# Performance work log

Measured on AMD Instinct MI355X. Metric: run time of the kernel, lower is better.

Reference implementation:

```python
import jax, jax.numpy as jnp
import numpy as np

# sarModule stage: in=256, out=512, blocks=2, stride=2, patch_groups=4, mask_size=7
B, C_IN, H, W = 32, 256, 56, 56
C_OUT = 512
PLANES = C_OUT // 4   # Bottleneck inner width = planes // expansion = 128
G = 4                 # patch_groups
MS = 7                # mask_size
TEMP = 1.0            # gumbel-softmax temperature


def conv(x, w, stride=1, pad=0, groups=1):
    return jax.lax.conv_general_dilated(
        x, w, (stride, stride), [(pad, pad), (pad, pad)],
        feature_group_count=groups,
        dimension_numbers=('NCHW', 'OIHW', 'NCHW'))


def bn(x, g, b):
    # BatchNorm in inference form with running_mean=0, running_var=1 folded in
    return x * g[None, :, None, None] + b[None, :, None, None]


def avgpool3s2(x):
    # nn.AvgPool2d(3, stride=2, padding=1), count_include_pad=True
    s = jax.lax.reduce_window(x, 0.0, jax.lax.add, (1, 1, 3, 3), (1, 1, 2, 2),
                              [(0, 0), (0, 0), (1, 1), (1, 1)])
    return s / 9.0


def setup_inputs() -> dict:
    key = jax.random.key(0)
    ks = iter(jax.random.split(key, 64))

    def w(shape):
        fan_in = int(np.prod(shape[1:]))
        return jax.random.normal(next(ks), shape, jnp.float32) * np.float32((2.0 / fan_in) ** 0.5)

    ones = lambda n: jnp.ones((n,), jnp.float32)
    zeros = lambda n: jnp.zeros((n,), jnp.float32)

    x = jax.random.normal(next(ks), (B, C_IN, H, W), jnp.float32)
    u = jax.random.uniform(next(ks), (B, 2, G, MS, MS), jnp.float32, 1e-6, 1.0 - 1e-6)
    gumbel_noise = -jnp.log(-jnp.log(u))

    return dict(
        x=x, gumbel_noise=gumbel_noise,
        # base Bottleneck (256->512, stride 2, downsample = avgpool + 1x1 conv + bn)
        b_w1=w((PLANES, C_IN, 1, 1)), b_g1=ones(PLANES), b_b1=zeros(PLANES),
        b_w2=w((PLANES, PLANES, 3, 3)), b_g2=ones(PLANES), b_b2=zeros(PLANES),
        b_w3=w((C_OUT, PLANES, 1, 1)), b_g3=ones(C_OUT), b_b3=zeros(C_OUT),
        b_dw=w((C_OUT, C_IN, 1, 1)), b_dg=ones(C_OUT), b_db=zeros(C_OUT),
        # refine Bottleneck (256->512, stride 1, downsample = 1x1 conv + bn)
        r_w1=w((PLANES, C_IN, 1, 1)), r_g1=ones(PLANES), r_b1=zeros(PLANES),
        r_w2=w((PLANES, PLANES, 3, 3)), r_g2=ones(PLANES), r_b2=zeros(PLANES),
        r_w3=w((C_OUT, PLANES, 1, 1)), r_g3=ones(C_OUT), r_b3=zeros(C_OUT),
        r_dw=w((C_OUT, C_IN, 1, 1)), r_dg=ones(C_OUT), r_db=zeros(C_OUT),
        # maskGen: grouped 3x3 conv (512 -> 4*G), bn, pool, grouped 1x1 fc (4*G -> 2*G)
        m_w=w((4 * G, C_OUT // G, 3, 3)), m_g=ones(4 * G), m_b=zeros(4 * G),
        m_fcw=w((2 * G, 4, 1, 1)),
        m_fcb=jnp.concatenate([0.1 * ones(G), 5.0 * ones(G)]),  # bias init from maskGen
        # fusion Bottleneck (512->512, stride 2, downsample = avgpool only)
        f_w1=w((PLANES, C_OUT, 1, 1)), f_g1=ones(PLANES), f_b1=zeros(PLANES),
        f_w2=w((PLANES, PLANES, 3, 3)), f_g2=ones(PLANES), f_b2=zeros(PLANES),
        f_w3=w((C_OUT, PLANES, 1, 1)), f_g3=ones(C_OUT), f_b3=zeros(C_OUT),
    )


def reference(x, gumbel_noise,
              b_w1, b_g1, b_b1, b_w2, b_g2, b_b2, b_w3, b_g3, b_b3, b_dw, b_dg, b_db,
              r_w1, r_g1, r_b1, r_w2, r_g2, r_b2, r_w3, r_g3, r_b3, r_dw, r_dg, r_db,
              m_w, m_g, m_b, m_fcw, m_fcb,
              f_w1, f_g1, f_b1, f_w2, f_g2, f_b2, f_w3, f_g3, f_b3):
    # ---- base branch: Bottleneck stride 2, last_relu=False -> [B,512,28,28]
    o = jax.nn.relu(bn(conv(x, b_w1), b_g1, b_b1))
    o = jax.nn.relu(bn(conv(o, b_w2, stride=2, pad=1), b_g2, b_b2))
    o = bn(conv(o, b_w3), b_g3, b_b3)
    x_base = o + bn(conv(avgpool3s2(x), b_dw), b_dg, b_db)

    # ---- maskGen on x_base
    gmap = jax.nn.relu(bn(conv(x_base, m_w, pad=1, groups=G), m_g, m_b))      # [B,16,28,28]
    hb = x_base.shape[2] // MS                                                 # adaptive avgpool 28->7
    gmap = gmap.reshape(B, 4 * G, MS, hb, MS, hb).mean(axis=(3, 5))            # [B,16,7,7]
    logits = conv(gmap, m_fcw, groups=G) + m_fcb[None, :, None, None]          # [B,8,7,7]
    logits = logits.reshape(B, 2, G, MS, MS)                                   # view(B,2,groups,ms,ms)
    # hard gumbel-softmax over dim 1 with straight-through estimator
    y = jax.nn.softmax((logits + gumbel_noise) / TEMP, axis=1)
    hard = jax.nn.one_hot(jnp.argmax(y, axis=1), 2, axis=1, dtype=y.dtype)
    gates = hard + y - jax.lax.stop_gradient(y)
    mask = gates[:, 1]                                                         # [B,G,7,7]

    # nearest-upsample mask x8 and expand across each channel group
    mask_up = jnp.repeat(jnp.repeat(mask, H // MS, axis=-2), W // MS, axis=-1) # [B,G,56,56]
    mask_full = jnp.broadcast_to(mask_up[:, :, None], (B, G, C_OUT // G, H, W)).reshape(B, C_OUT, H, W)

    # ---- refine branch: Bottleneck stride 1, output gated by mask, last_relu=False
    o = jax.nn.relu(bn(conv(x, r_w1), r_g1, r_b1))
    o = jax.nn.relu(bn(conv(o, r_w2, pad=1), r_g2, r_b2))
    o = bn(conv(o, r_w3), r_g3, r_b3) * mask_full
    x_refine = o + bn(conv(x, r_dw), r_dg, r_db)                               # [B,512,56,56]

    # ---- fuse: bilinear upsample base to refine resolution (align_corners=False)
    x_base_up = jax.image.resize(x_base, (B, C_OUT, H, W), 'bilinear')
    fused = jax.nn.relu(x_base_up + x_refine)

    # ---- fusion Bottleneck: stride 2, downsample = avgpool only, last_relu=True
    o = jax.nn.relu(bn(conv(fused, f_w1), f_g1, f_b1))
    o = jax.nn.relu(bn(conv(o, f_w2, stride=2, pad=1), f_g2, f_b2))
    o = bn(conv(o, f_w3), f_g3, f_b3)
    out = jax.nn.relu(o + avgpool3s2(fused))                                   # [B,512,28,28]
    return out, mask
```

## Files before the change

### kernel.cpp

```cpp
#include <hip/hip_runtime.h>
#include <cstdint>

#define BB   32
#define CINX 256
#define HH   56
#define WW   56
#define HWX  3136
#define CO   512
#define PL   128
#define HP   28
#define WP   28
#define HWP  784
#define NG   4
#define MSZ  7

typedef unsigned short ushortT;
typedef unsigned int   uint32;
typedef __attribute__((ext_vector_type(8))) short short8;
typedef __attribute__((ext_vector_type(4))) float f32x4;

__device__ __forceinline__ ushortT f2bf(float f){
  uint32 u = __float_as_uint(f);
  u = (u + 0x7fffu + ((u >> 16) & 1u)) >> 16;
  return (ushortT)u;
}
__device__ __forceinline__ float bf2f(ushortT u){
  return __uint_as_float(((uint32)u) << 16);
}
__device__ __forceinline__ void split2(float v, ushortT& h, ushortT& lo){
  h = f2bf(v);
  lo = f2bf(v - bf2f(h));
}
__device__ __forceinline__ uint32 packu(ushortT a, ushortT b){
  return (uint32)a | ((uint32)b << 16);
}

typedef __attribute__((address_space(1))) const void g_void;
typedef __attribute__((address_space(3))) void l_void;
__device__ __forceinline__ void glds16(const ushortT* g, ushortT* l){
  __builtin_amdgcn_global_load_lds((g_void*)g, (l_void*)l, 16, 0, 0);
}

__device__ __forceinline__ void wsplit(float v, ushortT* dh, ushortT* dl, size_t i){
  ushortT h, lo; split2(v, h, lo); dh[i] = h; dl[i] = lo;
}

__global__ __launch_bounds__(256) void prep_w(
  const float* __restrict__ b_w1, const float* __restrict__ b_g1,
  const float* __restrict__ b_w2, const float* __restrict__ b_g2,
  const float* __restrict__ b_w3, const float* __restrict__ b_g3,
  const float* __restrict__ b_dw, const float* __restrict__ b_dg,
  const float* __restrict__ r_w1, const float* __restrict__ r_g1,
  const float* __restrict__ r_w2, const float* __restrict__ r_g2,
  const float* __restrict__ r_w3, const float* __restrict__ r_g3,
  const float* __restrict__ r_dw, const float* __restrict__ r_dg,
  const float* __restrict__ f_w1, const float* __restrict__ f_g1,
  const float* __restrict__ f_w2, const float* __restrict__ f_g2,
  const float* __restrict__ f_w3, const float* __restrict__ f_g3,
  const float* __restrict__ b_b1, const float* __restrict__ r_b1,
  ushortT* __restrict__ dh, ushortT* __restrict__ dl,
  ushortT* __restrict__ zp, float* __restrict__ biasC)
{
  const int idx = blockIdx.x*256 + threadIdx.x;
  switch (blockIdx.y){
    case 0: {
      if (idx >= 32768) return; int m = idx >> 8;
      wsplit(b_w1[idx]*b_g1[m], dh, dl, (size_t)0 + idx); } break;
    case 3: {
      if (idx >= 32768) return; int m = idx >> 8;
      wsplit(r_w1[idx]*r_g1[m], dh, dl, 32768 + (size_t)idx); } break;
    case 1: {
      if (idx >= 147456) return; int m = idx / 1152; int k = idx - m*1152;
      int tap = k >> 7, c = k & 127;
      wsplit(b_w2[((size_t)(m*128 + c))*9 + tap]*b_g2[m], dh, dl, 65536 + (size_t)idx); } break;
    case 2: {
      if (idx >= 196608) return; int m = idx / 384; int k = idx - m*384;
      float v = (k < 128) ? b_w3[m*128 + k]*b_g3[m] : b_dw[m*256 + (k-128)]*b_dg[m];
      wsplit(v, dh, dl, 212992 + (size_t)idx); } break;
    case 4: {
      if (idx >= 147456) return; int m = idx / 1152; int k = idx - m*1152;
      int tap = k >> 7, c = k & 127;
      wsplit(r_w2[((size_t)(m*128 + c))*9 + tap]*r_g2[m], dh, dl, 409600 + (size_t)idx); } break;
    case 5: {
      if (idx >= 196608) return; int m = idx / 384; int k = idx - m*384;
      float v = (k < 128) ? r_w3[m*128 + k]*r_g3[m] : r_dw[m*256 + (k-128)]*r_dg[m];
      wsplit(v, dh, dl, 557056 + (size_t)idx); } break;
    case 6: {
      if (idx >= 65536) return; int m = idx >> 9;
      wsplit(f_w1[idx]*f_g1[m], dh, dl, 753664 + (size_t)idx); } break;
    case 7: {
      if (idx >= 147456) return; int m = idx / 1152; int k = idx - m*1152;
      int tap = k >> 7, c = k & 127;
      wsplit(f_w2[((size_t)(m*128 + c))*9 + tap]*f_g2[m], dh, dl, 819200 + (size_t)idx); } break;
    case 8: {
      if (idx >= 65536) return; int m = idx >> 7;
      wsplit(f_w3[idx]*f_g3[m], dh, dl, 966656 + (size_t)idx); } break;
    case 9: {
      if (idx < 64) zp[idx] = 0;
      if (idx < 128) biasC[idx] = b_b1[idx];
      else if (idx < 256) biasC[idx] = r_b1[idx-128];
    } break;
  }
}

__global__ __launch_bounds__(256) void k_pool2(const float* __restrict__ x,
    ushortT* __restrict__ ph_, ushortT* __restrict__ pl_){
  __shared__ float s[16][17];
  const int p0 = blockIdx.x*16, c0 = blockIdx.y*16, bz = blockIdx.z;
  const int ci = threadIdx.x >> 4, pi = threadIdx.x & 15;
  {
    const int p = p0 + pi;
    const int oy = p / WP, ox = p - oy*WP;
    const float* src = x + ((size_t)bz*CINX + c0 + ci)*HWX;
    float sum = 0.f;
    #pragma unroll
    for (int dy=0; dy<3; dy++){
      int yy = 2*oy-1+dy;
      if ((unsigned)yy >= HH) continue;
      #pragma unroll
      for (int dx=0; dx<3; dx++){
        int xx = 2*ox-1+dx;
        if ((unsigned)xx >= WW) continue;
        sum += src[yy*WW + xx];
      }
    }
    s[ci][pi] = sum * (1.f/9.f);
  }
  __syncthreads();
  const int pr = threadIdx.x >> 4, cj = threadIdx.x & 15;
  float v = s[cj][pr];
  ushortT h, lo; split2(v, h, lo);
  size_t o = ((size_t)bz*HWP + p0 + pr)*CINX + c0 + cj;
  ph_[o] = h; pl_[o] = lo;
}

__global__ __launch_bounds__(256) void prep_x2(const float* __restrict__ x,
    ushortT* __restrict__ xh, ushortT* __restrict__ xl){
  __shared__ float s[16][17];
  const int p0 = blockIdx.x*16, c0 = blockIdx.y*16, bz = blockIdx.z;
  const int ci = threadIdx.x >> 4, pi = threadIdx.x & 15;
  s[ci][pi] = x[((size_t)bz*CINX + c0 + ci)*HWX + p0 + pi];
  __syncthreads();
  const int pr = threadIdx.x >> 4, cj = threadIdx.x & 15;
  float v = s[cj][pr];
  ushortT h, lo; split2(v, h, lo);
  size_t o = ((size_t)bz*HWX + p0 + pr)*CINX + c0 + cj;
  xh[o] = h; xl[o] = lo;
}

__global__ __launch_bounds__(256) void k_poolf(const ushortT* __restrict__ fzh,
    const ushortT* __restrict__ fzl, float* __restrict__ pf){
  const int pb = blockIdx.x, bz = blockIdx.y;
  const int psub = threadIdx.x >> 6;
  const int lane = threadIdx.x & 63;
  const int p = pb*4 + psub;
  const int oy = p / WP, ox = p - oy*WP;
  const int c = lane*8;
  float s[8] = {0.f,0.f,0.f,0.f,0.f,0.f,0.f,0.f};
  #pragma unroll
  for (int dy=0; dy<3; dy++){
    const int iy = 2*oy - 1 + dy;
    if ((unsigned)iy >= (unsigned)HH) continue;
    #pragma unroll
    for (int dx=0; dx<3; dx++){
      const int ix = 2*ox - 1 + dx;
      if ((unsigned)ix >= (unsigned)WW) continue;
      const size_t fi = ((size_t)bz*HWX + (size_t)(iy*WW + ix))*CO + c;
      uint4 hh = *(const uint4*)(fzh + fi);
      uint4 ll = *(const uint4*)(fzl + fi);
      ushortT hv[8], lv[8];
      *(uint4*)hv = hh; *(uint4*)lv = ll;
      #pragma unroll
      for (int j=0;j<8;j++) s[j] += bf2f(hv[j]) + bf2f(lv[j]);
    }
  }
  const size_t o = ((size_t)bz*HWP + p)*CO + c;
  float4 o0 = make_float4(s[0]*(1.f/9.f), s[1]*(1.f/9.f), s[2]*(1.f/9.f), s[3]*(1.f/9.f));
  float4 o1 = make_float4(s[4]*(1.f/9.f), s[5]*(1.f/9.f), s[6]*(1.f/9.f), s[7]*(1.f/9.f));
  *(float4*)(pf + o)     = o0;
  *(float4*)(pf + o + 4) = o1;
}

template<int KIND,int EPI,int S1F,int MT,int NWV,int DBUF,int SWAP,int GX,int GY,
         int STRIDE,int PAD,int HIN,int WIN,int WOUT,int NOUT,int C1,int C2,
         int BSTR1,int MTOT,int KTOT>
__global__ __launch_bounds__(NWV*64)
void gemm_bf3(const ushortT* __restrict__ wph, const ushortT* __restrict__ wpl,
              const ushortT* __restrict__ s1h, const ushortT* __restrict__ s1l,
              const ushortT* __restrict__ s2h, const ushortT* __restrict__ s2l,
              const float* __restrict__ xf32,
              const float* __restrict__ bias1, const float* __restrict__ bias2,
              const float* __restrict__ maskf, const float* __restrict__ xbase,
              const ushortT* __restrict__ zp,
              ushortT* __restrict__ oh, ushortT* __restrict__ ol,
              float* __restrict__ of32)
{
  constexpr int ACALLS  = MT/(16*NWV);
  constexpr int BCALLS2 = 8/NWV;
  constexpr int GLDS_PER = (ACALLS + BCALLS2)*2;
  constexpr bool GATHER1 = (KIND==0 && S1F==1);
  constexpr int BUFSZ = MT*64 + 8192;
  constexpr int WNs = (MT==256) ? 2 : (NWV==8 ? 4 : 2);
  constexpr int NF  = 128/(WNs*16);
  constexpr int T = GX*GY*BB;
  static_assert(T % 8 == 0, "grid not divisible by 8 XCDs");
  constexpr int QX = T/8;
  __shared__ ushortT smem[BUFSZ*(DBUF+1)];

  const int tid = threadIdx.x;
  const int lin = blockIdx.x;
  const int virt = (lin & 7)*QX + (lin >> 3);
  const int vx = virt % GX;
  const int vrest = virt / GX;
  const int vy = vrest % GY;
  const int bz = vrest / GY;
  const int nt = SWAP ? vy : vx;
  const int mt = SWAP ? vx : vy;
  const int l  = tid & 63, w = tid >> 6;
  const int wm = w / WNs, wn = w % WNs;

  size_t a_src[2]; int a_dst[2];
  #pragma unroll
  for (int c=0;c<ACALLS;c++){
    int s = (w*ACALLS + c)*64 + l;
    int row = s >> 2, slotm = s & 3;
    int logical = slotm ^ ((row >> 1) & 3);
    a_src[c] = (size_t)(mt*MT + row)*KTOT + logical*8;
    a_dst[c] = (w*ACALLS + c)*512;
  }

  int b_dst[2]; size_t b_base1[2], b_base2[2]; int b_klane[2];
  int b_oy[2], b_ox[2]; bool b_ok[2]; float b_mv[2];
  #pragma unroll
  for (int c=0;c<BCALLS2;c++){
    int s = (w*BCALLS2 + c)*64 + l;
    int row = s >> 2, slotm = s & 3;
    int logical = slotm ^ ((row >> 1) & 3);
    b_klane[c] = logical*8;
    b_dst[c] = (w*BCALLS2 + c)*512;
    int ngr = nt*128 + row;
    b_ok[c] = (ngr < NOUT);
    int oyv = ngr / WOUT, oxv = ngr - (ngr / WOUT)*WOUT;
    b_oy[c] = oyv; b_ox[c] = oxv;
    b_base1[c] = ((size_t)bz*NOUT + ngr)*BSTR1 + b_klane[c];
    b_base2[c] = ((size_t)bz*NOUT + ngr)*C2 + b_klane[c];
    b_mv[c] = 1.f;
    if (KIND == 3)
      b_mv[c] = b_ok[c] ? maskf[((size_t)(bz*NG + mt)*MSZ + (oyv>>3))*MSZ + (oxv>>3)] : 0.f;
  }

  const int sr = tid >> 1;
  const int hp = tid & 1;
  const int swz = (sr >> 1) & 3;
  const int lws0 = sr*32 + ((2*hp) ^ swz)*8;
  const int lws1 = sr*32 + ((2*hp + 1) ^ swz)*8;
  const int ng = nt*128 + sr;

  f32x4 acc[4][4];
  f32x4 zf = {0.f,0.f,0.f,0.f};
  #pragma unroll
  for (int i=0;i<4;i++)
    #pragma unroll
    for (int j=0;j<4;j++) acc[i][j] = zf;

  auto stagef = [&](int ks, ushortT* AHb, ushortT* ALb, ushortT* BHb, ushortT* BLb){
    const int k0 = ks*32;
    #pragma unroll
    for (int c=0;c<ACALLS;c++){
      glds16(wph + a_src[c] + k0, AHb + a_dst[c]);
      glds16(wpl + a_src[c] + k0, ALb + a_dst[c]);
    }
    if constexpr (GATHER1){
      if (tid < 256){
        uint4 b0 = make_uint4(0,0,0,0), b1v = b0, b2v = b0, b3v = b0;
        if (ng < NOUT){
          size_t fbase = ((size_t)bz*C1 + k0 + hp*16)*(size_t)NOUT + ng;
          ushortT h[16], lo[16];
          #pragma unroll
          for (int e=0;e<16;e++){ split2(xf32[fbase + (size_t)e*NOUT], h[e], lo[e]); }
          b0  = make_uint4(packu(h[0],h[1]),  packu(h[2],h[3]),  packu(h[4],h[5]),  packu(h[6],h[7]));
          b1v = make_uint4(packu(h[8],h[9]),  packu(h[10],h[11]),packu(h[12],h[13]),packu(h[14],h[15]));
          b2v = make_uint4(packu(lo[0],lo[1]),packu(lo[2],lo[3]),packu(lo[4],lo[5]),packu(lo[6],lo[7]));
          b3v = make_uint4(packu(lo[8],lo[9]),packu(lo[10],lo[11]),packu(lo[12],lo[13]),packu(lo[14],lo[15]));
        }
        *(uint4*)(BHb + lws0) = b0;  *(uint4*)(BHb + lws1) = b1v;
        *(uint4*)(BLb + lws0) = b2v; *(uint4*)(BLb + lws1) = b3v;
      }
    } else {
      #pragma unroll
      for (int c=0;c<BCALLS2;c++){
        const ushortT *sh, *sl;
        if constexpr (KIND == 0){
          bool ok = b_ok[c];
          size_t off = b_base1[c] + k0;
          sh = ok ? s1h + off : zp;  sl = ok ? s1l + off : zp;
        } else if constexpr (KIND == 1){
          const int tap = k0 >> 7;
          const int cb  = (k0 & 127);
          const int dy = tap/3, dx = tap - 3*(tap/3);
          int iy = b_oy[c]*STRIDE + dy - PAD;
          int ix = b_ox[c]*STRIDE + dx - PAD;
          bool ok = b_ok[c] && (unsigned)iy < (unsigned)HIN && (unsigned)ix < (unsigned)WIN;
          size_t off = ((size_t)bz*(HIN*WIN) + (size_t)(iy*WIN + ix))*BSTR1 + cb + b_klane[c];
          sh = ok ? s1h + off : zp;  sl = ok ? s1l + off : zp;
        } else {
          if (k0 < C1){
            bool ok = b_ok[c] && (KIND != 3 || b_mv[c] != 0.f);
            size_t off = b_base1[c] + k0;
            sh = ok ? s1h + off : zp;  sl = ok ? s1l + off : zp;
          } else {
            bool ok = b_ok[c];
            size_t off = b_base2[c] + (k0 - C1);
            sh = ok ? s2h + off : zp;  sl = ok ? s2l + off : zp;
          }
        }
        glds16(sh, BHb + b_dst[c]);
        glds16(sl, BLb + b_dst[c]);
      }
    }
  };

  auto computef = [&](const ushortT* AHb, const ushortT* ALb,
                      const ushortT* BHb, const ushortT* BLb){
    short8 bh[NF], bl[NF];
    #pragma unroll
    for (int nf=0; nf<NF; nf++){
      const int rr = wn*(NF*16) + nf*16 + (l & 15);
      const int ph = (l >> 4) ^ ((rr >> 1) & 3);
      bh[nf] = *(const short8*)(BHb + rr*32 + ph*8);
      bl[nf] = *(const short8*)(BLb + rr*32 + ph*8);
    }
    #pragma unroll
    for (int mf=0; mf<4; mf++){
      const int rr = wm*64 + mf*16 + (l & 15);
      const int ph = (l >> 4) ^ ((rr >> 1) & 3);
      short8 ah = *(const short8*)(AHb + rr*32 + ph*8);
      short8 al = *(const short8*)(ALb + rr*32 + ph*8);
      #pragma unroll
      for (int nf=0; nf<NF; nf++)
        acc[mf][nf] = __builtin_amdgcn_mfma_f32_16x16x32_bf16(ah, bh[nf], acc[mf][nf], 0,0,0);
      #pragma unroll
      for (int nf=0; nf<NF; nf++)
        acc[mf][nf] = __builtin_amdgcn_mfma_f32_16x16x32_bf16(ah, bl[nf], acc[mf][nf], 0,0,0);
      #pragma unroll
      for (int nf=0; nf<NF; nf++)
        acc[mf][nf] = __builtin_amdgcn_mfma_f32_16x16x32_bf16(al, bh[nf], acc[mf][nf], 0,0,0);
    }
  };

  const int NK = KTOT / 32;
  if constexpr (DBUF == 0){
    ushortT* AH  = smem;
    ushortT* AL  = smem + MT*32;
    ushortT* BHs = smem + MT*64;
    ushortT* BLs = smem + MT*64 + 4096;
    for (int ks=0; ks<NK; ks++){
      stagef(ks, AH, AL, BHs, BLs);
      __syncthreads();
      computef(AH, AL, BHs, BLs);
      __syncthreads();
    }
  } else {
    stagef(0, smem, smem + MT*32, smem + MT*64, smem + MT*64 + 4096);
    asm volatile("s_waitcnt vmcnt(0)" ::: "memory");
    __builtin_amdgcn_s_barrier();
    for (int ks=0; ks<NK; ks++){
      ushortT* cb = smem + (ks & 1)*BUFSZ;
      ushortT* nb = smem + ((ks & 1) ^ 1)*BUFSZ;
      if (ks + 1 < NK){
        stagef(ks + 1, nb, nb + MT*32, nb + MT*64, nb + MT*64 + 4096);
        if constexpr (GLDS_PER == 4)
          asm volatile("s_waitcnt vmcnt(4)" ::: "memory");
        else
          asm volatile("s_waitcnt vmcnt(8)" ::: "memory");
      } else {
        asm volatile("s_waitcnt vmcnt(0)" ::: "memory");
      }
      __builtin_amdgcn_sched_barrier(0);
      __builtin_amdgcn_s_barrier();
      computef(cb, cb + MT*32, cb + MT*64, cb + MT*64 + 4096);
      __builtin_amdgcn_s_barrier();
    }
  }

  const int mb0 = mt*MT + wm*64;
  const int nb0 = nt*128 + wn*(NF*16);

  #pragma unroll
  for (int nf=0; nf<NF; nf++){
    const int n = nb0 + nf*16 + (l & 15);
    if (n >= NOUT) continue;
    if constexpr (EPI == 0){
      const size_t ob = ((size_t)bz*NOUT + n)*MTOT;
      #pragma unroll
      for (int mf=0; mf<4; mf++){
        const int m0 = mb0 + mf*16 + (l>>4)*4;
        ushort4 hq, lq; ushortT h0, l0; float v;
        v = fmaxf(acc[mf][nf][0] + bias1[m0+0], 0.f); split2(v,h0,l0); hq.x=h0; lq.x=l0;
        v = fmaxf(acc[mf][nf][1] + bias1[m0+1], 0.f); split2(v,h0,l0); hq.y=h0; lq.y=l0;
        v = fmaxf(acc[mf][nf][2] + bias1[m0+2], 0.f); split2(v,h0,l0); hq.z=h0; lq.z=l0;
        v = fmaxf(acc[mf][nf][3] + bias1[m0+3], 0.f); split2(v,h0,l0); hq.w=h0; lq.w=l0;
        *(ushort4*)(oh + ob + m0) = hq;
        *(ushort4*)(ol + ob + m0) = lq;
      }
    } else if constexpr (EPI == 1){
      #pragma unroll
      for (int mf=0; mf<4; mf++){
        const int m0 = mb0 + mf*16 + (l>>4)*4;
        #pragma unroll
        for (int r=0;r<4;r++){
          const int m = m0 + r;
          of32[((size_t)bz*MTOT + m)*NOUT + n] = acc[mf][nf][r] + bias1[m] + bias2[m];
        }
      }
    } else if constexpr (EPI == 2){
      const int y = n / WOUT, x = n - (n / WOUT)*WOUT;
      const int grpw = (mt*MT + wm*64) >> 7;
      const float mvv = maskf[((size_t)(bz*NG + grpw)*MSZ + (y>>3))*MSZ + (x>>3)];
      const int iy = y >> 1, ix = x >> 1;
      int yA,yB,xA,xB; float wyA,wyB,wxA,wxB;
      if (y & 1){ yA=iy; wyA=0.75f; yB=(iy+1<HP)?iy+1:HP-1; wyB=0.25f; }
      else      { yA=(iy>0)?iy-1:0; wyA=0.25f; yB=iy; wyB=0.75f; }
      if (x & 1){ xA=ix; wxA=0.75f; xB=(ix+1<WP)?ix+1:WP-1; wxB=0.25f; }
      else      { xA=(ix>0)?ix-1:0; wxA=0.25f; xB=ix; wxB=0.75f; }
      const size_t ob = ((size_t)bz*NOUT + n)*MTOT;
      #pragma unroll
      for (int mf=0; mf<4; mf++){
        const int m0 = mb0 + mf*16 + (l>>4)*4;
        ushort4 hq, lq;
        #pragma unroll
        for (int r=0;r<4;r++){
          const int m = m0 + r;
          const float* xb = xbase + ((size_t)bz*MTOT + m)*HWP;
          float up = wyA*(wxA*xb[yA*WP+xA] + wxB*xb[yA*WP+xB])
                   + wyB*(wxA*xb[yB*WP+xA] + wxB*xb[yB*WP+xB]);
          float v = fmaxf(acc[mf][nf][r] + up + mvv*bias1[m] + bias2[m], 0.f);
          ushortT h0, l0; split2(v, h0, l0);
          if      (r==0){hq.x=h0;lq.x=l0;}
          else if (r==1){hq.y=h0;lq.y=l0;}
          else if (r==2){hq.z=h0;lq.z=l0;}
          else          {hq.w=h0;lq.w=l0;}
        }
        *(ushort4*)(oh + ob + m0) = hq;
        *(ushort4*)(ol + ob + m0) = lq;
      }
    } else {
      const float* pfrow = xbase + ((size_t)bz*NOUT + n)*MTOT;
      #pragma unroll
      for (int mf=0; mf<4; mf++){
        const int m0 = mb0 + mf*16 + (l>>4)*4;
        const float4 pv = *(const float4*)(pfrow + m0);
        of32[((size_t)bz*MTOT + m0+0)*NOUT + n] = fmaxf(acc[mf][nf][0] + bias1[m0+0] + pv.x, 0.f);
        of32[((size_t)bz*MTOT + m0+1)*NOUT + n] = fmaxf(acc[mf][nf][1] + bias1[m0+1] + pv.y, 0.f);
        of32[((size_t)bz*MTOT + m0+2)*NOUT + n] = fmaxf(acc[mf][nf][2] + bias1[m0+2] + pv.z, 0.f);
        of32[((size_t)bz*MTOT + m0+3)*NOUT + n] = fmaxf(acc[mf][nf][3] + bias1[m0+3] + pv.w, 0.f);
      }
    }
  }
}

#define GM_LDSW 9216
__global__ __launch_bounds__(256) void k_gmap2(const float* __restrict__ xbase,
    const float* __restrict__ mw, const float* __restrict__ mg, const float* __restrict__ mb,
    float* __restrict__ gmap){
  __shared__ float wsh[GM_LDSW];
  __shared__ float red[16][2][4][16];
  const int tile = blockIdx.x, b = blockIdx.y;
  const int tid = threadIdx.x;
  const int pl = tid & 15, cs = tid >> 4;
  const int p = tile*16 + pl;
  const int oy = p / WP, ox = p - oy*WP;
  int toff[9];
  #pragma unroll
  for (int tap=0; tap<9; tap++){
    int dy = tap/3, dx = tap - 3*dy;
    int yy = oy + dy - 1, xx = ox + dx - 1;
    toff[tap] = ((unsigned)yy < (unsigned)HP && (unsigned)xx < (unsigned)WP) ? (yy*WP + xx) : -1;
  }
  float acc[2][4] = {{0.f,0.f,0.f,0.f},{0.f,0.f,0.f,0.f}};
  for (int pass=0; pass<2; pass++){
    __syncthreads();
    for (int i = tid; i < GM_LDSW; i += 256){
      int ocl = i & 3, tap = (i >> 2) % 9, c_rel = i / 36;
      int cg = pass*256 + c_rel;
      int g = cg >> 7;
      int oc = g*4 + ocl;
      wsh[i] = mw[((size_t)(oc*128 + (cg & 127)))*9 + tap] * mg[oc];
    }
    __syncthreads();
    const float* xb = xbase + ((size_t)b*CO + pass*256 + cs*16)*HWP;
    for (int cl=0; cl<16; cl++){
      const float* xc = xb + (size_t)cl*HWP;
      const float* wr = &wsh[(cs*16 + cl)*36];
      #pragma unroll
      for (int tap=0; tap<9; tap++){
        if (toff[tap] < 0) continue;
        float v = xc[toff[tap]];
        f32x4 w4 = *(const f32x4*)(wr + tap*4);
        acc[pass][0] += v*w4[0];
        acc[pass][1] += v*w4[1];
        acc[pass][2] += v*w4[2];
        acc[pass][3] += v*w4[3];
      }
    }
  }
  #pragma unroll
  for (int pp=0; pp<2; pp++)
    #pragma unroll
    for (int o=0; o<4; o++)
      red[cs][pp][o][pl] = acc[pp][o];
  __syncthreads();
  const int oc = tid >> 4;
  const int g = oc >> 2, ocl = oc & 3, pg = g >> 1, cs0 = (g & 1)*8;
  float s = 0.f;
  #pragma unroll
  for (int t=0; t<8; t++) s += red[cs0 + t][pg][ocl][pl];
  s = fmaxf(s + mb[oc], 0.f);
  gmap[((size_t)b*16 + oc)*HWP + p] = s;
}

__global__ __launch_bounds__(256) void k_gpool(const float* __restrict__ gmap, float* __restrict__ gpool){
  int idx = blockIdx.x*256 + threadIdx.x;
  if (idx >= BB*16*49) return;
  int q = idx % 49; int t = idx / 49; int ch = t % 16; int b = t / 16;
  int my = q/7, mx = q%7;
  const float* src = gmap + ((size_t)b*16 + ch)*HWP;
  float s = 0.f;
  #pragma unroll
  for (int yb=0;yb<4;yb++)
    #pragma unroll
    for (int xb=0;xb<4;xb++)
      s += src[(my*4+yb)*WP + (mx*4+xb)];
  gpool[idx] = s * (1.f/16.f);
}

__global__ __launch_bounds__(256) void k_mask(const float* __restrict__ gpool, const float* __restrict__ fcw,
    const float* __restrict__ fcb, const float* __restrict__ gum,
    float* __restrict__ maskf, float* __restrict__ mout){
  int idx = blockIdx.x*256 + threadIdx.x;
  if (idx >= BB*NG*49) return;
  int q = idx % 49; int t = idx / 49; int g = t % NG; int b = t / NG;
  float lgt[2];
  #pragma unroll
  for (int cls=0; cls<2; cls++){
    int c = cls*NG + g;
    int gc = c >> 1;
    float s = fcb[c];
    #pragma unroll
    for (int k=0;k<4;k++)
      s += fcw[c*4+k] * gpool[((size_t)b*16 + gc*4 + k)*49 + q];
    s += gum[(((size_t)b*2 + cls)*NG + g)*49 + q];
    lgt[cls] = s;
  }
  float m = (lgt[1] > lgt[0]) ? 1.f : 0.f;
  maskf[idx] = m;
  mout[idx] = m;
}

extern "C" void kernel_launch(void* const* d_in, const int* in_sizes, int n_in,
                              void* d_out, int out_size, void* d_ws, size_t ws_size,
                              hipStream_t stream){
  const float* x    = (const float*)d_in[0];
  const float* gum  = (const float*)d_in[1];
  const float* b_w1 = (const float*)d_in[2];
  const float* b_g1 = (const float*)d_in[3];
  const float* b_b1 = (const float*)d_in[4];
  const float* b_w2 = (const float*)d_in[5];
  const float* b_g2 = (const float*)d_in[6];
  const float* b_b2 = (const float*)d_in[7];
  const float* b_w3 = (const float*)d_in[8];
  const float* b_g3 = (const float*)d_in[9];
  const float* b_b3 = (const float*)d_in[10];
  const float* b_dw = (const float*)d_in[11];
  const float* b_dg = (const float*)d_in[12];
  const float* b_db = (const float*)d_in[13];
  const float* r_w1 = (const float*)d_in[14];
  const float* r_g1 = (const float*)d_in[15];
  const float* r_b1 = (const float*)d_in[16];
  const float* r_w2 = (const float*)d_in[17];
  const float* r_g2 = (const float*)d_in[18];
  const float* r_b2 = (const float*)d_in[19];
  const float* r_w3 = (const float*)d_in[20];
  const float* r_g3 = (const float*)d_in[21];
  const float* r_b3 = (const float*)d_in[22];
  const float* r_dw = (const float*)d_in[23];
  const float* r_dg = (const float*)d_in[24];
  const float* r_db = (const float*)d_in[25];
  const float* m_w  = (const float*)d_in[26];
  const float* m_g  = (const float*)d_in[27];
  const float* m_b  = (const float*)d_in[28];
  const float* m_fcw= (const float*)d_in[29];
  const float* m_fcb= (const float*)d_in[30];
  const float* f_w1 = (const float*)d_in[31];
  const float* f_g1 = (const float*)d_in[32];
  const float* f_b1 = (const float*)d_in[33];
  const float* f_w2 = (const float*)d_in[34];
  const float* f_g2 = (const float*)d_in[35];
  const float* f_b2 = (const float*)d_in[36];
  const float* f_w3 = (const float*)d_in[37];
  const float* f_g3 = (const float*)d_in[38];
  const float* f_b3 = (const float*)d_in[39];

  char* ws = (char*)d_ws;
  constexpr size_t O_WPH  = 0;
  constexpr size_t O_WPL  = 2064384;
  constexpr size_t O_CH   = 4128768;
  constexpr size_t O_DH   = 55508992;
  constexpr size_t O_DL   = 61931520;
  constexpr size_t O_EH   = 68354048;
  constexpr size_t O_EL   = 94044160;
  constexpr size_t O_PF   = O_EH;
  constexpr size_t O_XB   = 119734272;
  constexpr size_t O_GMAP = 171114496;
  constexpr size_t O_GPOOL= 172720128;
  constexpr size_t O_MASK = 172820480;
  constexpr size_t O_FH   = 172845568;
  constexpr size_t O_PH   = 172845568;
  constexpr size_t O_PL   = 185690624;
  constexpr size_t O_FL   = 275606016;
  constexpr size_t O_ZP   = 378366464;
  constexpr size_t O_BIASC= 378366592;

  ushortT* WPH = (ushortT*)(ws + O_WPH);
  ushortT* WPL = (ushortT*)(ws + O_WPL);
  ushortT* MGH = (ushortT*)(ws + O_CH);
  ushortT* XH  = (ushortT*)(ws + O_CH);
  ushortT* F1H = (ushortT*)(ws + O_CH);
  ushortT* F1L = (ushortT*)(ws + O_CH + 25690112);
  ushortT* DHp = (ushortT*)(ws + O_DH);
  ushortT* DLp = (ushortT*)(ws + O_DL);
  ushortT* EHp = (ushortT*)(ws + O_EH);
  ushortT* ELp = (ushortT*)(ws + O_EL);
  float*   PF  = (float*)(ws + O_PF);
  float*   XB  = (float*)(ws + O_XB);
  ushortT* PHp = (ushortT*)(ws + O_PH);
  ushortT* PLp = (ushortT*)(ws + O_PL);
  ushortT* FHp = (ushortT*)(ws + O_FH);
  ushortT* FLp = (ushortT*)(ws + O_FL);
  float*   GMAP = (float*)(ws + O_GMAP);
  float*   GPOOL= (float*)(ws + O_GPOOL);
  float*   MASKF= (float*)(ws + O_MASK);
  ushortT* ZP  = (ushortT*)(ws + O_ZP);
  float*   BIASC = (float*)(ws + O_BIASC);
  (void)ws_size;

  float* outp = (float*)d_out;
  float* mout = outp + (size_t)BB*CO*HWP;
  ushortT* dout_u = (ushortT*)d_out;

  dim3 blk(256), blk512(512);
  const ushortT* nu = nullptr; const float* nf_ = nullptr;
  ushortT* nuo = nullptr; float* nfo = nullptr;

  prep_w<<<dim3(768, 10), blk, 0, stream>>>(b_w1,b_g1,b_w2,b_g2,b_w3,b_g3,b_dw,b_dg,
      r_w1,r_g1,r_w2,r_g2,r_w3,r_g3,r_dw,r_dg,f_w1,f_g1,f_w2,f_g2,f_w3,f_g3,
      b_b1, r_b1, WPH, WPL, ZP, BIASC);
  k_pool2<<<dim3(49, 16, BB), blk, 0, stream>>>(x, PHp, PLp);

  gemm_bf3<0,0,1,256,8,0,0, 25,1, 1,0,56,56,56,3136, 256,0,256, 256,256><<<dim3(800), blk512, 0, stream>>>(
      WPH+0, WPL+0, nu, nu, nu, nu, x, BIASC, nf_, nf_, nf_, ZP, MGH, dout_u, nfo);
  gemm_bf3<1,0,0,128,8,1,0, 7,1, 2,1,56,56,28,784, 128,0,256, 128,1152><<<dim3(224), blk512, 0, stream>>>(
      WPH+65536, WPL+65536, MGH, dout_u, nu, nu, nf_, b_b2, nf_, nf_, nf_, ZP, DHp, DLp, nfo);
  gemm_bf3<2,1,0,256,8,0,0, 7,2, 1,0,28,28,28,784, 128,256,128, 512,384><<<dim3(448), blk512, 0, stream>>>(
      WPH+212992, WPL+212992, DHp, DLp, PHp, PLp, nf_, b_b3, b_db, nf_, nf_, ZP, nuo, nuo, XB);

  k_gmap2<<<dim3(49, BB), blk, 0, stream>>>(XB, m_w, m_g, m_b, GMAP);
  k_gpool<<<dim3(98), blk, 0, stream>>>(GMAP, GPOOL);
  k_mask<<<dim3(25), blk, 0, stream>>>(GPOOL, m_fcw, m_fcb, gum, MASKF, mout);

  gemm_bf3<1,0,0,128,8,1,0, 25,1, 1,1,56,56,56,3136, 128,0,256, 128,1152><<<dim3(800), blk512, 0, stream>>>(
      WPH+409600, WPL+409600, MGH+128, dout_u+128, nu, nu, nf_, r_b2, nf_, nf_, nf_, ZP, EHp, ELp, nfo);

  prep_x2<<<dim3(196, 16, BB), blk, 0, stream>>>(x, XH, dout_u);

  gemm_bf3<3,2,0,128,8,1,1, 4,25, 1,0,56,56,56,3136, 128,256,128, 512,384><<<dim3(3200), blk512, 0, stream>>>(
      WPH+557056, WPL+557056, EHp, ELp, XH, dout_u, nf_, r_b3, r_db, MASKF, XB, ZP, FHp, FLp, nfo);

  k_poolf<<<dim3(196, BB), blk, 0, stream>>>(FHp, FLp, PF);

  gemm_bf3<0,0,0,128,8,1,0, 25,1, 1,0,56,56,56,3136, 512,0,512, 128,512><<<dim3(800), blk512, 0, stream>>>(
      WPH+753664, WPL+753664, FHp, FLp, nu, nu, nf_, f_b1, nf_, nf_, nf_, ZP, F1H, F1L, nfo);
  gemm_bf3<1,0,0,128,8,1,0, 7,1, 2,1,56,56,28,784, 128,0,128, 128,1152><<<dim3(224), blk512, 0, stream>>>(
      WPH+819200, WPL+819200, F1H, F1L, nu, nu, nf_, f_b2, nf_, nf_, nf_, ZP, DHp, DLp, nfo);
  gemm_bf3<0,3,0,256,8,0,0, 7,2, 1,0,28,28,28,784, 128,0,128, 512,128><<<dim3(448), blk512, 0, stream>>>(
      WPH+966656, WPL+966656, DHp, DLp, nu, nu, nf_, f_b3, nf_, nf_, PF, ZP, nuo, nuo, outp);
}
```

Before: 1.051 ms.

## Use 4-wave blocks for MT=128 GEMMs, spread fp32 gather, raise MFMA priority

Five of the GEMM launches that use a 128-row tile drop from 8 waves (512 threads) to 4 waves (256 threads), so each wave computes more output fragments. The fp32 gather path is redistributed so that every thread loads and splits 8 elements instead of half the threads handling 16. A vmcnt(6) wait variant is added for the new per-thread load count. s_setprio is raised around the MFMA loop to favour issuing matrix instructions. The intent is fewer idle waves and better per-wave reuse, at the cost of higher register pressure and possibly lower occupancy.

```diff
diff --git a/kernel.cpp b/kernel.cpp
--- a/kernel.cpp
+++ b/kernel.cpp
@@ -249,12 +249,11 @@
       b_mv[c] = b_ok[c] ? maskf[((size_t)(bz*NG + mt)*MSZ + (oyv>>3))*MSZ + (oxv>>3)] : 0.f;
   }
 
-  const int sr = tid >> 1;
-  const int hp = tid & 1;
-  const int swz = (sr >> 1) & 3;
-  const int lws0 = sr*32 + ((2*hp) ^ swz)*8;
-  const int lws1 = sr*32 + ((2*hp + 1) ^ swz)*8;
-  const int ng = nt*128 + sr;
+  const int g_sr = tid >> 2;
+  const int g_hq = tid & 3;
+  const int g_swz = (g_sr >> 1) & 3;
+  const int g_lws = g_sr*32 + (g_hq ^ g_swz)*8;
+  const int g_ng = nt*128 + g_sr;
 
   f32x4 acc[4][4];
   f32x4 zf = {0.f,0.f,0.f,0.f};
@@ -271,21 +270,17 @@
       glds16(wpl + a_src[c] + k0, ALb + a_dst[c]);
     }
     if constexpr (GATHER1){
-      if (tid < 256){
-        uint4 b0 = make_uint4(0,0,0,0), b1v = b0, b2v = b0, b3v = b0;
-        if (ng < NOUT){
-          size_t fbase = ((size_t)bz*C1 + k0 + hp*16)*(size_t)NOUT + ng;
-          ushortT h[16], lo[16];
-          #pragma unroll
-          for (int e=0;e<16;e++){ split2(xf32[fbase + (size_t)e*NOUT], h[e], lo[e]); }
-          b0  = make_uint4(packu(h[0],h[1]),  packu(h[2],h[3]),  packu(h[4],h[5]),  packu(h[6],h[7]));
-          b1v = make_uint4(packu(h[8],h[9]),  packu(h[10],h[11]),packu(h[12],h[13]),packu(h[14],h[15]));
-          b2v = make_uint4(packu(lo[0],lo[1]),packu(lo[2],lo[3]),packu(lo[4],lo[5]),packu(lo[6],lo[7]));
-          b3v = make_uint4(packu(lo[8],lo[9]),packu(lo[10],lo[11]),packu(lo[12],lo[13]),packu(lo[14],lo[15]));
-        }
-        *(uint4*)(BHb + lws0) = b0;  *(uint4*)(BHb + lws1) = b1v;
-        *(uint4*)(BLb + lws0) = b2v; *(uint4*)(BLb + lws1) = b3v;
-      }
+      uint4 bh4 = make_uint4(0,0,0,0), bl4 = bh4;
+      if (g_ng < NOUT){
+        size_t fbase = ((size_t)bz*C1 + k0 + g_hq*8)*(size_t)NOUT + g_ng;
+        ushortT h[8], lo[8];
+        #pragma unroll
+        for (int e=0;e<8;e++){ split2(xf32[fbase + (size_t)e*NOUT], h[e], lo[e]); }
+        bh4 = make_uint4(packu(h[0],h[1]),  packu(h[2],h[3]),  packu(h[4],h[5]),  packu(h[6],h[7]));
+        bl4 = make_uint4(packu(lo[0],lo[1]),packu(lo[2],lo[3]),packu(lo[4],lo[5]),packu(lo[6],lo[7]));
+      }
+      *(uint4*)(BHb + g_lws) = bh4;
+      *(uint4*)(BLb + g_lws) = bl4;
     } else {
       #pragma unroll
       for (int c=0;c<BCALLS2;c++){
@@ -330,6 +325,7 @@
       bh[nf] = *(const short8*)(BHb + rr*32 + ph*8);
       bl[nf] = *(const short8*)(BLb + rr*32 + ph*8);
     }
+    __builtin_amdgcn_s_setprio(1);
     #pragma unroll
     for (int mf=0; mf<4; mf++){
       const int rr = wm*64 + mf*16 + (l & 15);
@@ -346,6 +342,7 @@
       for (int nf=0; nf<NF; nf++)
         acc[mf][nf] = __builtin_amdgcn_mfma_f32_16x16x32_bf16(al, bh[nf], acc[mf][nf], 0,0,0);
     }
+    __builtin_amdgcn_s_setprio(0);
   };
 
   const int NK = KTOT / 32;
@@ -371,6 +368,8 @@
         stagef(ks + 1, nb, nb + MT*32, nb + MT*64, nb + MT*64 + 4096);
         if constexpr (GLDS_PER == 4)
           asm volatile("s_waitcnt vmcnt(4)" ::: "memory");
+        else if constexpr (GLDS_PER == 6)
+          asm volatile("s_waitcnt vmcnt(6)" ::: "memory");
         else
           asm volatile("s_waitcnt vmcnt(8)" ::: "memory");
       } else {
@@ -659,7 +658,7 @@
 
   gemm_bf3<0,0,1,256,8,0,0, 25,1, 1,0,56,56,56,3136, 256,0,256, 256,256><<<dim3(800), blk512, 0, stream>>>(
       WPH+0, WPL+0, nu, nu, nu, nu, x, BIASC, nf_, nf_, nf_, ZP, MGH, dout_u, nfo);
-  gemm_bf3<1,0,0,128,8,1,0, 7,1, 2,1,56,56,28,784, 128,0,256, 128,1152><<<dim3(224), blk512, 0, stream>>>(
+  gemm_bf3<1,0,0,128,4,1,0, 7,1, 2,1,56,56,28,784, 128,0,256, 128,1152><<<dim3(224), blk, 0, stream>>>(
       WPH+65536, WPL+65536, MGH, dout_u, nu, nu, nf_, b_b2, nf_, nf_, nf_, ZP, DHp, DLp, nfo);
   gemm_bf3<2,1,0,256,8,0,0, 7,2, 1,0,28,28,28,784, 128,256,128, 512,384><<<dim3(448), blk512, 0, stream>>>(
       WPH+212992, WPL+212992, DHp, DLp, PHp, PLp, nf_, b_b3, b_db, nf_, nf_, ZP, nuo, nuo, XB);
@@ -668,19 +667,19 @@
   k_gpool<<<dim3(98), blk, 0, stream>>>(GMAP, GPOOL);
   k_mask<<<dim3(25), blk, 0, stream>>>(GPOOL, m_fcw, m_fcb, gum, MASKF, mout);
 
-  gemm_bf3<1,0,0,128,8,1,0, 25,1, 1,1,56,56,56,3136, 128,0,256, 128,1152><<<dim3(800), blk512, 0, stream>>>(
+  gemm_bf3<1,0,0,128,4,1,0, 25,1, 1,1,56,56,56,3136, 128,0,256, 128,1152><<<dim3(800), blk, 0, stream>>>(
       WPH+409600, WPL+409600, MGH+128, dout_u+128, nu, nu, nf_, r_b2, nf_, nf_, nf_, ZP, EHp, ELp, nfo);
 
   prep_x2<<<dim3(196, 16, BB), blk, 0, stream>>>(x, XH, dout_u);
 
-  gemm_bf3<3,2,0,128,8,1,1, 4,25, 1,0,56,56,56,3136, 128,256,128, 512,384><<<dim3(3200), blk512, 0, stream>>>(
+  gemm_bf3<3,2,0,128,4,1,1, 4,25, 1,0,56,56,56,3136, 128,256,128, 512,384><<<dim3(3200), blk, 0, stream>>>(
       WPH+557056, WPL+557056, EHp, ELp, XH, dout_u, nf_, r_b3, r_db, MASKF, XB, ZP, FHp, FLp, nfo);
 
   k_poolf<<<dim3(196, BB), blk, 0, stream>>>(FHp, FLp, PF);
 
-  gemm_bf3<0,0,0,128,8,1,0, 25,1, 1,0,56,56,56,3136, 512,0,512, 128,512><<<dim3(800), blk512, 0, stream>>>(
+  gemm_bf3<0,0,0,128,4,1,0, 25,1, 1,0,56,56,56,3136, 512,0,512, 128,512><<<dim3(800), blk, 0, stream>>>(
       WPH+753664, WPL+753664, FHp, FLp, nu, nu, nf_, f_b1, nf_, nf_, nf_, ZP, F1H, F1L, nfo);
-  gemm_bf3<1,0,0,128,8,1,0, 7,1, 2,1,56,56,28,784, 128,0,128, 128,1152><<<dim3(224), blk512, 0, stream>>>(
+  gemm_bf3<1,0,0,128,4,1,0, 7,1, 2,1,56,56,28,784, 128,0,128, 128,1152><<<dim3(224), blk, 0, stream>>>(
       WPH+819200, WPL+819200, F1H, F1L, nu, nu, nf_, f_b2, nf_, nf_, nf_, ZP, DHp, DLp, nfo);
   gemm_bf3<0,3,0,256,8,0,0, 7,2, 1,0,28,28,28,784, 128,0,128, 512,128><<<dim3(448), blk512, 0, stream>>>(
       WPH+966656, WPL+966656, DHp, DLp, nu, nu, nf_, f_b3, nf_, nf_, PF, ZP, nuo, nuo, outp);
```

After: 1.053 ms. Within noise of the previous version (+0.2%).
